# Optimization experiments

Hardware: AMD Instinct MI355X
Metric: run time of the kernel (lower is better)

Reference implementation:

```python
import jax, jax.numpy as jnp
import numpy as np

N = 100000   # nodes
E = 1600000  # edges
G = 512      # graphs
IN_F = 128
HID = 64
EPS = 1e-5


def setup_inputs() -> dict:
    key = jax.random.key(0)
    ks = jax.random.split(key, 16)
    x = jax.random.normal(ks[0], (N, IN_F), dtype=jnp.float32)
    edge_index = jax.random.randint(ks[1], (2, E), 0, N, dtype=jnp.int64)
    batch = jnp.sort(jax.random.randint(ks[2], (N,), 0, G, dtype=jnp.int64))
    s = 0.05
    return {
        'x': x, 'edge_index': edge_index, 'batch': batch,
        'W1': jax.random.normal(ks[3], (IN_F, HID), jnp.float32) * s,
        'b1': jax.random.normal(ks[4], (HID,), jnp.float32) * s,
        'g1': jax.random.uniform(ks[5], (HID,), jnp.float32),
        'be1': jax.random.normal(ks[6], (HID,), jnp.float32) * s,
        'rm1': jnp.zeros((HID,), jnp.float32),
        'rv1': jnp.ones((HID,), jnp.float32),
        'W2': jax.random.normal(ks[7], (HID, HID), jnp.float32) * s,
        'b2': jax.random.normal(ks[8], (HID,), jnp.float32) * s,
        'g2': jax.random.uniform(ks[9], (HID,), jnp.float32),
        'be2': jax.random.normal(ks[10], (HID,), jnp.float32) * s,
        'rm2': jnp.zeros((HID,), jnp.float32),
        'rv2': jnp.ones((HID,), jnp.float32),
        'Wh1': jax.random.normal(ks[11], (2 * HID, HID), jnp.float32) * s,
        'bh1': jax.random.normal(ks[12], (HID,), jnp.float32) * s,
        'Wh2': jax.random.normal(ks[13], (HID, HID // 2), jnp.float32) * s,
        'bh2': jnp.zeros((HID // 2,), jnp.float32),
        'Wh3': jax.random.normal(ks[14], (HID // 2, 1), jnp.float32) * s,
        'bh3': jnp.zeros((1,), jnp.float32),
    }


def _gcn(h, W, b, src, dst):
    # GCNConv with added self-loops and symmetric D^{-1/2} A D^{-1/2} normalization
    hw = h @ W                                   # [N, HID]
    deg = jnp.ones((N,), hw.dtype).at[dst].add(1.0)  # in-degree + self-loop
    dinv = jax.lax.rsqrt(deg)
    norm = dinv[src] * dinv[dst]                 # [E]
    agg = jax.ops.segment_sum(hw[src] * norm[:, None], dst, num_segments=N)
    return agg + hw * (dinv * dinv)[:, None] + b  # self-loop term + bias


def _bn(x, g, b, rm, rv):
    return (x - rm) * jax.lax.rsqrt(rv + EPS) * g + b


def reference(x, edge_index, batch, W1, b1, g1, be1, rm1, rv1,
              W2, b2, g2, be2, rm2, rv2, Wh1, bh1, Wh2, bh2, Wh3, bh3):
    src, dst = edge_index[0], edge_index[1]
    # layer 0 (no residual: dim change 128 -> 64)
    h = jax.nn.relu(_bn(_gcn(x, W1, b1, src, dst), g1, be1, rm1, rv1))
    # layer 1 with residual
    h = h + jax.nn.relu(_bn(_gcn(h, W2, b2, src, dst), g2, be2, rm2, rv2))
    # global mean + max pooling per graph
    ones = jnp.ones((N,), h.dtype)
    cnt = jnp.maximum(jax.ops.segment_sum(ones, batch, num_segments=G), 1.0)
    h_mean = jax.ops.segment_sum(h, batch, num_segments=G) / cnt[:, None]
    h_max = jax.ops.segment_max(h, batch, num_segments=G)
    hg = jnp.concatenate([h_mean, h_max], axis=-1)   # [G, 2*HID]
    # MLP head (dropout disabled in eval)
    z = jax.nn.relu(hg @ Wh1 + bh1)
    z = jax.nn.relu(z @ Wh2 + bh2)
    out = z @ Wh3 + bh3
    return jax.nn.sigmoid(out).squeeze(-1)           # [G]
```

## Files before the change

### kernel.cpp

```cpp
#include <hip/hip_runtime.h>
#include <math.h>

#define NN 100000
#define EE 1600000
#define GG 512
#define INF_ 128
#define HID 64
#define EPS 1e-5f

#define NBUK 391
#define P1_TILES 98
#define SETUP_B 25
#define POOL_WORDS (GG * 64 * 2 + GG)
#define ZERO_B ((POOL_WORDS + 255) / 256)

typedef unsigned int uint32;
typedef __attribute__((ext_vector_type(8))) short bf16x8;
typedef __attribute__((ext_vector_type(4))) float f32x4;

static __device__ inline uint32 f2bf(float f) {
    uint32 u = __float_as_uint(f);
    return (u + 0x7FFFu + ((u >> 16) & 1u)) >> 16;
}
static __device__ inline float bf_lo(uint32 u) { return __uint_as_float(u << 16); }
static __device__ inline float bf_hi(uint32 u) { return __uint_as_float(u & 0xFFFF0000u); }


__global__ __launch_bounds__(256) void k_hist1(const int* __restrict__ ei,
        int* __restrict__ hblk,
        const float* b1, const float* g1, const float* be1,
        const float* rm1, const float* rv1,
        const float* b2, const float* g2, const float* be2,
        const float* rm2, const float* rv2, float* sc,
        const float* W1, uint32* Wt1b, const float* W2, uint32* Wt2b,
        float* poolz) {
    int b = blockIdx.x, t = threadIdx.x;
    if (b < P1_TILES) {
        __shared__ int h[NBUK];
        for (int i = t; i < NBUK; i += 256) h[i] = 0;
        __syncthreads();
        const int4* dst4 = (const int4*)(ei + EE);
        int base4 = b * 4096;
        for (int j = 0; j < 16; ++j) {
            int i4 = base4 + j * 256 + t;
            if (i4 < EE / 4) {
                int4 d = dst4[i4];
                atomicAdd(&h[d.x >> 8], 1);
                atomicAdd(&h[d.y >> 8], 1);
                atomicAdd(&h[d.z >> 8], 1);
                atomicAdd(&h[d.w >> 8], 1);
            }
        }
        __syncthreads();
        for (int i = t; i < NBUK; i += 256) hblk[b * NBUK + i] = h[i];
    } else if (b < P1_TILES + SETUP_B) {
        int i = (b - P1_TILES) * 256 + t;
        if (i < 4096) {
            int n = i >> 6, kp = (i & 63) * 2;
            Wt1b[i] = f2bf(W1[(size_t)kp * 64 + n]) |
                      (f2bf(W1[(size_t)(kp + 1) * 64 + n]) << 16);
        } else if (i < 6144) {
            int j = i - 4096;
            int n = j >> 5, kp = (j & 31) * 2;
            Wt2b[j] = f2bf(W2[(size_t)kp * 64 + n]) |
                      (f2bf(W2[(size_t)(kp + 1) * 64 + n]) << 16);
        } else if (i < 6208) {
            int l = i - 6144;
            float s1 = g1[l] * rsqrtf(rv1[l] + EPS);
            sc[l]       = s1;
            sc[64 + l]  = (b1[l] - rm1[l]) * s1 + be1[l];
            float s2 = g2[l] * rsqrtf(rv2[l] + EPS);
            sc[128 + l] = s2;
            sc[192 + l] = (b2[l] - rm2[l]) * s2 + be2[l];
        }
    } else {
        int i = (b - P1_TILES - SETUP_B) * 256 + t;
        if (i < POOL_WORDS) poolz[i] = 0.f;
    }
}

__global__ void k_scan2(const int* __restrict__ hblk, int* __restrict__ bbase,
                        int* __restrict__ rbase, int* __restrict__ offs) {
    __shared__ int wsum[8];
    int t = threadIdx.x;
    int lane = t & 63, w = t >> 6;
    int c = 0;
    if (t < NBUK)
        for (int b = 0; b < P1_TILES; ++b) c += hblk[b * NBUK + t];
    int v = c;
    for (int d = 1; d < 64; d <<= 1) { int n = __shfl_up(v, d); if (lane >= d) v += n; }
    if (lane == 63) wsum[w] = v;
    __syncthreads();
    int pre = 0;
    for (int q = 0; q < w; ++q) pre += wsum[q];
    int excl = pre + v - c;
    if (t <= NBUK) bbase[t] = excl;
    if (t == 0) offs[NN] = EE;
    if (t < NBUK) {
        int run = excl;
        for (int b = 0; b < P1_TILES; ++b) {
            rbase[b * NBUK + t] = run;
            run += hblk[b * NBUK + t];
        }
    }
}

__global__ __launch_bounds__(256) void k_p1b(const int* __restrict__ ei,
                                             const int* __restrict__ rbase,
                                             uint32* __restrict__ pairs) {
    __shared__ int h[NBUK];
    int b = blockIdx.x, t = threadIdx.x;
    for (int i = t; i < NBUK; i += 256) h[i] = rbase[b * NBUK + i];
    __syncthreads();
    const int4* src4 = (const int4*)ei;
    const int4* dst4 = (const int4*)(ei + EE);
    int base4 = b * 4096;
    for (int j = 0; j < 16; ++j) {
        int i4 = base4 + j * 256 + t;
        if (i4 < EE / 4) {
            int4 d = dst4[i4];
            int4 s = src4[i4];
            int p0 = atomicAdd(&h[d.x >> 8], 1);
            pairs[p0] = ((uint32)s.x << 8) | (uint32)(d.x & 255);
            int p1 = atomicAdd(&h[d.y >> 8], 1);
            pairs[p1] = ((uint32)s.y << 8) | (uint32)(d.y & 255);
            int p2 = atomicAdd(&h[d.z >> 8], 1);
            pairs[p2] = ((uint32)s.z << 8) | (uint32)(d.z & 255);
            int p3 = atomicAdd(&h[d.w >> 8], 1);
            pairs[p3] = ((uint32)s.w << 8) | (uint32)(d.w & 255);
        }
    }
}

__global__ __launch_bounds__(256) void k_p2(const uint32* __restrict__ pairs,
                                            const int* __restrict__ bbase,
                                            int* __restrict__ offs, float* __restrict__ dinv,
                                            int* __restrict__ col) {
    int b = blockIdx.x, t = threadIdx.x;
    int nbase = b << 8;
    int ebase = bbase[b], eend = bbase[b + 1];
    int m = eend - ebase;
    __shared__ int cnt[256];
    __shared__ int wsum[4];
    cnt[t] = 0;
    __syncthreads();
    for (int i = t; i < m; i += 256)
        atomicAdd(&cnt[pairs[ebase + i] & 255u], 1);
    __syncthreads();
    int c = cnt[t];
    int lane = t & 63, w = t >> 6;
    int v = c;
    for (int d = 1; d < 64; d <<= 1) { int n = __shfl_up(v, d); if (lane >= d) v += n; }
    if (lane == 63) wsum[w] = v;
    __syncthreads();
    int pre = 0;
    for (int q = 0; q < w; ++q) pre += wsum[q];
    int excl = pre + v - c;
    int node = nbase + t;
    if (node < NN) {
        offs[node] = ebase + excl;
        dinv[node] = rsqrtf(1.f + (float)c);
    }
    __syncthreads();
    cnt[t] = excl;
    __syncthreads();
    for (int i = t; i < m; i += 256) {
        uint32 u = pairs[ebase + i];
        int loc = atomicAdd(&cnt[u & 255u], 1);
        col[ebase + loc] = (int)(u >> 8);
    }
}

template <int K>
__global__ __launch_bounds__(256) void k_gemm_mfma(const float* __restrict__ X,
                                                   const uint32* __restrict__ Wtb,
                                                   uint32* __restrict__ outb, int nrows) {
    constexpr int KP = K + 8;
    __shared__ alignas(16) unsigned short Al[64 * KP];
    __shared__ alignas(16) unsigned short Bl[64 * KP];
    int tid = threadIdx.x;
    for (int i = tid; i < 64 * (K / 2); i += 256) {
        int n = i / (K / 2), kp = i % (K / 2);
        *(uint32*)&Bl[n * KP + kp * 2] = Wtb[i];
    }
    int r0 = blockIdx.x * 64;
    const float* Xb = X + (size_t)r0 * K;
    int limit = (nrows - r0) * K;
    for (int f = tid * 4; f < 64 * K; f += 1024) {
        float4 v = {0.f, 0.f, 0.f, 0.f};
        if (f + 3 < limit) v = *(const float4*)&Xb[f];
        int row = f / K, kpos = f % K;
        ushort4 pk;
        pk.x = (unsigned short)f2bf(v.x);
        pk.y = (unsigned short)f2bf(v.y);
        pk.z = (unsigned short)f2bf(v.z);
        pk.w = (unsigned short)f2bf(v.w);
        *(ushort4*)&Al[row * KP + kpos] = pk;
    }
    __syncthreads();
    int lane = tid & 63, wv = tid >> 6;
    int m = lane & 15, quad = lane >> 4;
    f32x4 acc0 = {0.f, 0.f, 0.f, 0.f}, acc1 = acc0, acc2 = acc0, acc3 = acc0;
    int arow = wv * 16 + m;
#pragma unroll
    for (int k0 = 0; k0 < K; k0 += 32) {
        int koff = k0 + quad * 8;
        bf16x8 a = *(const bf16x8*)&Al[arow * KP + koff];
        bf16x8 b0 = *(const bf16x8*)&Bl[(0 * 16 + m) * KP + koff];
        bf16x8 b1 = *(const bf16x8*)&Bl[(1 * 16 + m) * KP + koff];
        bf16x8 b2 = *(const bf16x8*)&Bl[(2 * 16 + m) * KP + koff];
        bf16x8 b3 = *(const bf16x8*)&Bl[(3 * 16 + m) * KP + koff];
        acc0 = __builtin_amdgcn_mfma_f32_16x16x32_bf16(a, b0, acc0, 0, 0, 0);
        acc1 = __builtin_amdgcn_mfma_f32_16x16x32_bf16(a, b1, acc1, 0, 0, 0);
        acc2 = __builtin_amdgcn_mfma_f32_16x16x32_bf16(a, b2, acc2, 0, 0, 0);
        acc3 = __builtin_amdgcn_mfma_f32_16x16x32_bf16(a, b3, acc3, 0, 0, 0);
    }
    const float* accs[4] = {(const float*)&acc0, (const float*)&acc1,
                            (const float*)&acc2, (const float*)&acc3};
#pragma unroll
    for (int nt = 0; nt < 4; ++nt) {
#pragma unroll
        for (int reg = 0; reg < 4; ++reg) {
            float val = accs[nt][reg];
            float nxt = __shfl_down(val, 1);
            int row = r0 + wv * 16 + quad * 4 + reg;
            if (((m & 1) == 0) && row < nrows)
                outb[(size_t)row * 32 + nt * 8 + (m >> 1)] =
                    f2bf(val) | (f2bf(nxt) << 16);
        }
    }
}

__global__ void k_gcn_gather(const uint32* __restrict__ hwb, const int* __restrict__ col,
                             const int* __restrict__ offs,
                             const float* __restrict__ dinv, const float* __restrict__ scale,
                             const float* __restrict__ shift, const float* __restrict__ resid,
                             float* __restrict__ out) {
    int node = blockIdx.x * 4 + (threadIdx.x >> 6);
    if (node >= NN) return;
    int lane = threadIdx.x & 63;
    int half = lane >> 5;
    int fl = lane & 31;
    int e0 = offs[node], e1 = offs[node + 1];
    float di = dinv[node];
    float ax0 = 0.f, ay0 = 0.f, ax1 = 0.f, ay1 = 0.f;
    for (int base = e0; base < e1; base += 64) {
        int m = e1 - base; if (m > 64) m = 64;
        int srcv = 0; float wv = 0.f;
        if (lane < m) { srcv = col[base + lane]; wv = dinv[srcv]; }
        for (int j = 0; j < m; j += 16) {
            int   s0 = __shfl(srcv, j + half);
            int   s1 = __shfl(srcv, j + 2 + half);
            int   s2 = __shfl(srcv, j + 4 + half);
            int   s3 = __shfl(srcv, j + 6 + half);
            int   s4 = __shfl(srcv, j + 8 + half);
            int   s5 = __shfl(srcv, j + 10 + half);
            int   s6 = __shfl(srcv, j + 12 + half);
            int   s7 = __shfl(srcv, j + 14 + half);
            float w0 = __shfl(wv, j + half);
            float w1 = __shfl(wv, j + 2 + half);
            float w2 = __shfl(wv, j + 4 + half);
            float w3 = __shfl(wv, j + 6 + half);
            float w4 = __shfl(wv, j + 8 + half);
            float w5 = __shfl(wv, j + 10 + half);
            float w6 = __shfl(wv, j + 12 + half);
            float w7 = __shfl(wv, j + 14 + half);
            uint32 u0 = hwb[(size_t)s0 * 32 + fl];
            uint32 u1 = hwb[(size_t)s1 * 32 + fl];
            uint32 u2 = hwb[(size_t)s2 * 32 + fl];
            uint32 u3 = hwb[(size_t)s3 * 32 + fl];
            uint32 u4 = hwb[(size_t)s4 * 32 + fl];
            uint32 u5 = hwb[(size_t)s5 * 32 + fl];
            uint32 u6 = hwb[(size_t)s6 * 32 + fl];
            uint32 u7 = hwb[(size_t)s7 * 32 + fl];
            ax0 = fmaf(bf_lo(u0), w0, ax0); ay0 = fmaf(bf_hi(u0), w0, ay0);
            ax1 = fmaf(bf_lo(u1), w1, ax1); ay1 = fmaf(bf_hi(u1), w1, ay1);
            ax0 = fmaf(bf_lo(u2), w2, ax0); ay0 = fmaf(bf_hi(u2), w2, ay0);
            ax1 = fmaf(bf_lo(u3), w3, ax1); ay1 = fmaf(bf_hi(u3), w3, ay1);
            ax0 = fmaf(bf_lo(u4), w4, ax0); ay0 = fmaf(bf_hi(u4), w4, ay0);
            ax1 = fmaf(bf_lo(u5), w5, ax1); ay1 = fmaf(bf_hi(u5), w5, ay1);
            ax0 = fmaf(bf_lo(u6), w6, ax0); ay0 = fmaf(bf_hi(u6), w6, ay0);
            ax1 = fmaf(bf_lo(u7), w7, ax1); ay1 = fmaf(bf_hi(u7), w7, ay1);
        }
    }
    float ax = ax0 + ax1, ay = ay0 + ay1;
    ax += __shfl(ax, fl + 32);
    ay += __shfl(ay, fl + 32);
    if (half == 0) {
        uint32 uself = hwb[(size_t)node * 32 + fl];
        float dii = di * di;
        float vx = fmaf(ax * di + bf_lo(uself) * dii, scale[2 * fl],     shift[2 * fl]);
        float vy = fmaf(ay * di + bf_hi(uself) * dii, scale[2 * fl + 1], shift[2 * fl + 1]);
        vx = fmaxf(vx, 0.f);
        vy = fmaxf(vy, 0.f);
        if (resid) {
            float2 rv = *(const float2*)&resid[(size_t)node * 64 + 2 * fl];
            vx += rv.x; vy += rv.y;
        }
        float2 o; o.x = vx; o.y = vy;
        *(float2*)&out[(size_t)node * 64 + 2 * fl] = o;
    }
}

__global__ __launch_bounds__(256) void k_pool(const float* __restrict__ h,
                       const int* __restrict__ batch,
                       float* __restrict__ msum, float* __restrict__ mmax,
                       float* __restrict__ gcnt) {
    int lane = threadIdx.x & 63;
    int wv = threadIdx.x >> 6;
    int i0 = blockIdx.x * 128 + wv * 32;
    if (i0 >= NN) return;
    int i1 = i0 + 32; if (i1 > NN) i1 = NN;
    int cur = batch[i0];
    float sum = 0.f, mx = 0.f; int c = 0;
    for (int i = i0; i < i1; ++i) {
        int g = batch[i];
        if (g != cur) {
            atomicAdd(&msum[cur * 64 + lane], sum);
            atomicMax((unsigned int*)&mmax[cur * 64 + lane], __float_as_uint(mx));
            if (lane == 0) atomicAdd(&gcnt[cur], (float)c);
            sum = 0.f; mx = 0.f; c = 0; cur = g;
        }
        float v = h[(long)i * 64 + lane];
        sum += v; mx = fmaxf(mx, v); ++c;
    }
    atomicAdd(&msum[cur * 64 + lane], sum);
    atomicMax((unsigned int*)&mmax[cur * 64 + lane], __float_as_uint(mx));
    if (lane == 0) atomicAdd(&gcnt[cur], (float)c);
}

__global__ void k_head(const float* __restrict__ msum, const float* __restrict__ mmax,
                       const float* __restrict__ gcnt,
                       const float* __restrict__ Wh1, const float* __restrict__ bh1,
                       const float* __restrict__ Wh2, const float* __restrict__ bh2,
                       const float* __restrict__ Wh3, const float* __restrict__ bh3,
                       float* __restrict__ out) {
    int g = blockIdx.x, t = threadIdx.x;
    __shared__ float hg[128];
    __shared__ float z1[64];
    __shared__ float z2[32];
    float c = fmaxf(gcnt[g], 1.f);
    hg[t]      = msum[g * 64 + t] / c;
    hg[64 + t] = mmax[g * 64 + t];
    __syncthreads();
    float acc = bh1[t];
#pragma unroll 8
    for (int k = 0; k < 128; ++k) acc = fmaf(hg[k], Wh1[k * 64 + t], acc);
    z1[t] = fmaxf(acc, 0.f);
    __syncthreads();
    if (t < 32) {
        float a2 = bh2[t];
#pragma unroll 8
        for (int k = 0; k < 64; ++k) a2 = fmaf(z1[k], Wh2[k * 32 + t], a2);
        z2[t] = fmaxf(a2, 0.f);
    }
    __syncthreads();
    if (t == 0) {
        float a3 = bh3[0];
        for (int k = 0; k < 32; ++k) a3 = fmaf(z2[k], Wh3[k], a3);
        out[g] = 1.f / (1.f + expf(-a3));
    }
}


static inline size_t alignup(size_t x) { return (x + 255) & ~(size_t)255; }

extern "C" void kernel_launch(void* const* d_in, const int* in_sizes, int n_in,
                              void* d_out, int out_size, void* d_ws, size_t ws_size,
                              hipStream_t stream) {
    const float* x   = (const float*)d_in[0];
    const int*   ei  = (const int*)d_in[1];
    const int*   bat = (const int*)d_in[2];
    const float* W1  = (const float*)d_in[3];
    const float* b1  = (const float*)d_in[4];
    const float* g1  = (const float*)d_in[5];
    const float* be1 = (const float*)d_in[6];
    const float* rm1 = (const float*)d_in[7];
    const float* rv1 = (const float*)d_in[8];
    const float* W2  = (const float*)d_in[9];
    const float* b2  = (const float*)d_in[10];
    const float* g2  = (const float*)d_in[11];
    const float* be2 = (const float*)d_in[12];
    const float* rm2 = (const float*)d_in[13];
    const float* rv2 = (const float*)d_in[14];
    const float* Wh1 = (const float*)d_in[15];
    const float* bh1 = (const float*)d_in[16];
    const float* Wh2 = (const float*)d_in[17];
    const float* bh2 = (const float*)d_in[18];
    const float* Wh3 = (const float*)d_in[19];
    const float* bh3 = (const float*)d_in[20];
    float* out = (float*)d_out;

    char* ws = (char*)d_ws;
    size_t o = 0;
    int*   hblk   = (int*)(ws + o);  o = alignup(o + (size_t)P1_TILES * NBUK * 4);
    int*   rbase  = (int*)(ws + o);  o = alignup(o + (size_t)P1_TILES * NBUK * 4);
    int*   bbase  = (int*)(ws + o);  o = alignup(o + (NBUK + 1) * 4);
    int*   offs   = (int*)(ws + o);  o = alignup(o + (NN + 1) * 4);
    uint32* pairs = (uint32*)(ws + o); o = alignup(o + (size_t)EE * 4);
    int*   col    = (int*)(ws + o);  o = alignup(o + (size_t)EE * 4);
    float* dinv   = (float*)(ws + o); o = alignup(o + (size_t)NN * 4);
    float* scb    = (float*)(ws + o); o = alignup(o + 4 * 64 * 4);
    uint32* Wt1b  = (uint32*)(ws + o); o = alignup(o + 64 * (INF_ / 2) * 4);
    uint32* Wt2b  = (uint32*)(ws + o); o = alignup(o + 64 * (HID / 2) * 4);
    float* msum   = (float*)(ws + o); o += (size_t)GG * 64 * 4;
    float* mmax   = (float*)(ws + o); o += (size_t)GG * 64 * 4;
    float* gcnt   = (float*)(ws + o); o += (size_t)GG * 4;
    o = alignup(o);
    uint32* hwb   = (uint32*)(ws + o); o = alignup(o + (size_t)NN * 32 * 4);
    float* h      = (float*)(ws + o); o = alignup(o + (size_t)NN * 64 * 4);
    (void)ws_size; (void)n_in; (void)in_sizes; (void)out_size;

    k_hist1<<<P1_TILES + SETUP_B + ZERO_B, 256, 0, stream>>>(
        ei, hblk, b1, g1, be1, rm1, rv1, b2, g2, be2, rm2, rv2, scb,
        W1, Wt1b, W2, Wt2b, msum);
    k_scan2<<<1, 512, 0, stream>>>(hblk, bbase, rbase, offs);
    k_p1b<<<P1_TILES, 256, 0, stream>>>(ei, rbase, pairs);
    k_p2<<<NBUK, 256, 0, stream>>>(pairs, bbase, offs, dinv, col);

    k_gemm_mfma<INF_><<<(NN + 63) / 64, 256, 0, stream>>>(x, Wt1b, hwb, NN);
    k_gcn_gather<<<(NN + 3) / 4, 256, 0, stream>>>(hwb, col, offs, dinv,
                                                   scb, scb + 64, nullptr, h);
    k_gemm_mfma<HID><<<(NN + 63) / 64, 256, 0, stream>>>(h, Wt2b, hwb, NN);
    k_gcn_gather<<<(NN + 3) / 4, 256, 0, stream>>>(hwb, col, offs, dinv,
                                                   scb + 128, scb + 192, h, h);
    k_pool<<<(NN + 127) / 128, 256, 0, stream>>>(h, bat, msum, mmax, gcnt);
    k_head<<<GG, 64, 0, stream>>>(msum, mmax, gcnt, Wh1, bh1, Wh2, bh2, Wh3, bh3, out);
}
```

Measured before the change: 306.6 us.

## Prescale GEMM output by dinv and simplify gather to unweighted sums

The GEMM epilogue now multiplies each row by dinv[row], so the stored features are already source-normalised. The gather no longer loads dinv per neighbour or shuffles weights; it loads 16 column indices directly per iteration, which are wave-uniform, and sums features without weights. The self-loop and destination scaling are folded into a single multiply by di, and col is padded with 16 zeroed entries so the tail reads stay in bounds. This removes a dependent gather of dinv and many shuffles, at the cost of rounding the prescaled values to bf16 and issuing redundant scalar or broadcast index loads.

```diff
diff --git a/kernel.cpp b/kernel.cpp
--- a/kernel.cpp
+++ b/kernel.cpp
@@ -80,10 +80,12 @@
 }
 
 __global__ void k_scan2(const int* __restrict__ hblk, int* __restrict__ bbase,
-                        int* __restrict__ rbase, int* __restrict__ offs) {
+                        int* __restrict__ rbase, int* __restrict__ offs,
+                        int* __restrict__ col) {
     __shared__ int wsum[8];
     int t = threadIdx.x;
     int lane = t & 63, w = t >> 6;
+    if (t < 16) col[EE + t] = 0;
     int c = 0;
     if (t < NBUK)
         for (int b = 0; b < P1_TILES; ++b) c += hblk[b * NBUK + t];
@@ -174,6 +176,7 @@
 template <int K>
 __global__ __launch_bounds__(256) void k_gemm_mfma(const float* __restrict__ X,
                                                    const uint32* __restrict__ Wtb,
+                                                   const float* __restrict__ dinv,
                                                    uint32* __restrict__ outb, int nrows) {
     constexpr int KP = K + 8;
     __shared__ alignas(16) unsigned short Al[64 * KP];
@@ -215,13 +218,19 @@
         acc2 = __builtin_amdgcn_mfma_f32_16x16x32_bf16(a, b2, acc2, 0, 0, 0);
         acc3 = __builtin_amdgcn_mfma_f32_16x16x32_bf16(a, b3, acc3, 0, 0, 0);
     }
+    float dv[4];
+#pragma unroll
+    for (int reg = 0; reg < 4; ++reg) {
+        int row = r0 + wv * 16 + quad * 4 + reg;
+        dv[reg] = (row < nrows) ? dinv[row] : 0.f;
+    }
     const float* accs[4] = {(const float*)&acc0, (const float*)&acc1,
                             (const float*)&acc2, (const float*)&acc3};
 #pragma unroll
     for (int nt = 0; nt < 4; ++nt) {
 #pragma unroll
         for (int reg = 0; reg < 4; ++reg) {
-            float val = accs[nt][reg];
+            float val = accs[nt][reg] * dv[reg];
             float nxt = __shfl_down(val, 1);
             int row = r0 + wv * 16 + quad * 4 + reg;
             if (((m & 1) == 0) && row < nrows)
@@ -234,63 +243,55 @@
 __global__ void k_gcn_gather(const uint32* __restrict__ hwb, const int* __restrict__ col,
                              const int* __restrict__ offs,
                              const float* __restrict__ dinv, const float* __restrict__ scale,
-                             const float* __restrict__ shift, const float* __restrict__ resid,
-                             float* __restrict__ out) {
-    int node = blockIdx.x * 4 + (threadIdx.x >> 6);
+                             const float* __restrict__ shift, const float* resid,
+                             float* out) {
+    int wid = __builtin_amdgcn_readfirstlane((int)(threadIdx.x >> 6));
+    int node = blockIdx.x * 4 + wid;
     if (node >= NN) return;
-    int lane = threadIdx.x & 63;
+    int lane = (int)(threadIdx.x & 63);
     int half = lane >> 5;
     int fl = lane & 31;
     int e0 = offs[node], e1 = offs[node + 1];
     float di = dinv[node];
+    uint32 uself = hwb[(uint32)node * 32u + (uint32)fl];
     float ax0 = 0.f, ay0 = 0.f, ax1 = 0.f, ay1 = 0.f;
-    for (int base = e0; base < e1; base += 64) {
-        int m = e1 - base; if (m > 64) m = 64;
-        int srcv = 0; float wv = 0.f;
-        if (lane < m) { srcv = col[base + lane]; wv = dinv[srcv]; }
-        for (int j = 0; j < m; j += 16) {
-            int   s0 = __shfl(srcv, j + half);
-            int   s1 = __shfl(srcv, j + 2 + half);
-            int   s2 = __shfl(srcv, j + 4 + half);
-            int   s3 = __shfl(srcv, j + 6 + half);
-            int   s4 = __shfl(srcv, j + 8 + half);
-            int   s5 = __shfl(srcv, j + 10 + half);
-            int   s6 = __shfl(srcv, j + 12 + half);
-            int   s7 = __shfl(srcv, j + 14 + half);
-            float w0 = __shfl(wv, j + half);
-            float w1 = __shfl(wv, j + 2 + half);
-            float w2 = __shfl(wv, j + 4 + half);
-            float w3 = __shfl(wv, j + 6 + half);
-            float w4 = __shfl(wv, j + 8 + half);
-            float w5 = __shfl(wv, j + 10 + half);
-            float w6 = __shfl(wv, j + 12 + half);
-            float w7 = __shfl(wv, j + 14 + half);
-            uint32 u0 = hwb[(size_t)s0 * 32 + fl];
-            uint32 u1 = hwb[(size_t)s1 * 32 + fl];
-            uint32 u2 = hwb[(size_t)s2 * 32 + fl];
-            uint32 u3 = hwb[(size_t)s3 * 32 + fl];
-            uint32 u4 = hwb[(size_t)s4 * 32 + fl];
-            uint32 u5 = hwb[(size_t)s5 * 32 + fl];
-            uint32 u6 = hwb[(size_t)s6 * 32 + fl];
-            uint32 u7 = hwb[(size_t)s7 * 32 + fl];
-            ax0 = fmaf(bf_lo(u0), w0, ax0); ay0 = fmaf(bf_hi(u0), w0, ay0);
-            ax1 = fmaf(bf_lo(u1), w1, ax1); ay1 = fmaf(bf_hi(u1), w1, ay1);
-            ax0 = fmaf(bf_lo(u2), w2, ax0); ay0 = fmaf(bf_hi(u2), w2, ay0);
-            ax1 = fmaf(bf_lo(u3), w3, ax1); ay1 = fmaf(bf_hi(u3), w3, ay1);
-            ax0 = fmaf(bf_lo(u4), w4, ax0); ay0 = fmaf(bf_hi(u4), w4, ay0);
-            ax1 = fmaf(bf_lo(u5), w5, ax1); ay1 = fmaf(bf_hi(u5), w5, ay1);
-            ax0 = fmaf(bf_lo(u6), w6, ax0); ay0 = fmaf(bf_hi(u6), w6, ay0);
-            ax1 = fmaf(bf_lo(u7), w7, ax1); ay1 = fmaf(bf_hi(u7), w7, ay1);
+    for (int base = e0; base < e1; base += 16) {
+        const int* cp = col + base;
+        int m = e1 - base;
+        int s[16];
+#pragma unroll
+        for (int j = 0; j < 16; ++j) s[j] = cp[j];
+        if (m >= 16) {
+            uint32 u[8];
+#pragma unroll
+            for (int p = 0; p < 8; ++p) {
+                int sv = half ? s[2 * p + 1] : s[2 * p];
+                u[p] = hwb[(uint32)sv * 32u + (uint32)fl];
+            }
+#pragma unroll
+            for (int p = 0; p < 8; ++p) {
+                if (p & 1) { ax1 += bf_lo(u[p]); ay1 += bf_hi(u[p]); }
+                else       { ax0 += bf_lo(u[p]); ay0 += bf_hi(u[p]); }
+            }
+        } else {
+#pragma unroll
+            for (int p = 0; p < 8; ++p) {
+                if (2 * p < m) {
+                    int sv = half ? s[2 * p + 1] : s[2 * p];
+                    float w = (2 * p + half < m) ? 1.f : 0.f;
+                    uint32 u = hwb[(uint32)sv * 32u + (uint32)fl];
+                    ax0 = fmaf(bf_lo(u), w, ax0);
+                    ay0 = fmaf(bf_hi(u), w, ay0);
+                }
+            }
         }
     }
     float ax = ax0 + ax1, ay = ay0 + ay1;
     ax += __shfl(ax, fl + 32);
     ay += __shfl(ay, fl + 32);
     if (half == 0) {
-        uint32 uself = hwb[(size_t)node * 32 + fl];
-        float dii = di * di;
-        float vx = fmaf(ax * di + bf_lo(uself) * dii, scale[2 * fl],     shift[2 * fl]);
-        float vy = fmaf(ay * di + bf_hi(uself) * dii, scale[2 * fl + 1], shift[2 * fl + 1]);
+        float vx = fmaf((ax + bf_lo(uself)) * di, scale[2 * fl],     shift[2 * fl]);
+        float vy = fmaf((ay + bf_hi(uself)) * di, scale[2 * fl + 1], shift[2 * fl + 1]);
         vx = fmaxf(vx, 0.f);
         vy = fmaxf(vy, 0.f);
         if (resid) {
@@ -398,7 +399,7 @@
     int*   bbase  = (int*)(ws + o);  o = alignup(o + (NBUK + 1) * 4);
     int*   offs   = (int*)(ws + o);  o = alignup(o + (NN + 1) * 4);
     uint32* pairs = (uint32*)(ws + o); o = alignup(o + (size_t)EE * 4);
-    int*   col    = (int*)(ws + o);  o = alignup(o + (size_t)EE * 4);
+    int*   col    = (int*)(ws + o);  o = alignup(o + (size_t)(EE + 16) * 4);
     float* dinv   = (float*)(ws + o); o = alignup(o + (size_t)NN * 4);
     float* scb    = (float*)(ws + o); o = alignup(o + 4 * 64 * 4);
     uint32* Wt1b  = (uint32*)(ws + o); o = alignup(o + 64 * (INF_ / 2) * 4);
@@ -414,14 +415,14 @@
     k_hist1<<<P1_TILES + SETUP_B + ZERO_B, 256, 0, stream>>>(
         ei, hblk, b1, g1, be1, rm1, rv1, b2, g2, be2, rm2, rv2, scb,
         W1, Wt1b, W2, Wt2b, msum);
-    k_scan2<<<1, 512, 0, stream>>>(hblk, bbase, rbase, offs);
+    k_scan2<<<1, 512, 0, stream>>>(hblk, bbase, rbase, offs, col);
     k_p1b<<<P1_TILES, 256, 0, stream>>>(ei, rbase, pairs);
     k_p2<<<NBUK, 256, 0, stream>>>(pairs, bbase, offs, dinv, col);
 
-    k_gemm_mfma<INF_><<<(NN + 63) / 64, 256, 0, stream>>>(x, Wt1b, hwb, NN);
+    k_gemm_mfma<INF_><<<(NN + 63) / 64, 256, 0, stream>>>(x, Wt1b, dinv, hwb, NN);
     k_gcn_gather<<<(NN + 3) / 4, 256, 0, stream>>>(hwb, col, offs, dinv,
                                                    scb, scb + 64, nullptr, h);
-    k_gemm_mfma<HID><<<(NN + 63) / 64, 256, 0, stream>>>(h, Wt2b, hwb, NN);
+    k_gemm_mfma<HID><<<(NN + 63) / 64, 256, 0, stream>>>(h, Wt2b, dinv, hwb, NN);
     k_gcn_gather<<<(NN + 3) / 4, 256, 0, stream>>>(hwb, col, offs, dinv,
                                                    scb + 128, scb + 192, h, h);
     k_pool<<<(NN + 127) / 128, 256, 0, stream>>>(h, bat, msum, mmax, gcnt);
```

Result: slower. 640.2 us (+108.8%).
